# Optimization experiments

Hardware: AMD Instinct MI355X
Metric: run time of the kernel (lower is better)

The kernel has to match this reference:

```python
import jax, jax.numpy as jnp
import numpy as np

N_DELAYS = 512
N_SAMPLES = 2 ** 15  # 32768


def _interp_linear(x, out_size):
    # F.interpolate(mode='linear', align_corners=False) on [B, C, L]
    L = x.shape[-1]
    scale = L / out_size
    pos = (jnp.arange(out_size, dtype=jnp.float32) + 0.5) * scale - 0.5
    pos = jnp.clip(pos, 0.0, L - 1)
    i0 = jnp.floor(pos).astype(jnp.int32)
    i1 = jnp.minimum(i0 + 1, L - 1)
    w = (pos - i0).astype(x.dtype)
    return x[..., i0] * (1.0 - w) + x[..., i1] * w


def _interp_nearest(x, out_size):
    # F.interpolate(mode='nearest') on [B, C, L]: idx = floor(j * L/out)
    L = x.shape[-1]
    idx = jnp.clip(jnp.floor(jnp.arange(out_size) * (L / out_size)).astype(jnp.int32), 0, L - 1)
    return x[..., idx]


def setup_inputs() -> dict:
    key = jax.random.key(0)
    k1, k2, k3, k4, k5 = jax.random.split(key, 5)
    batch = 8
    impulse = jax.random.normal(k1, (batch, 128), dtype=jnp.float32)
    delay_selection = jax.random.normal(k2, (batch, N_DELAYS, 16), dtype=jnp.float32)
    damping = jax.random.normal(k3, (batch, 1), dtype=jnp.float32)
    filt = jax.random.normal(k4, (batch, 16), dtype=jnp.float32)
    # torch forward draws uniform(-1,1) noise; passed as input for determinism
    noise = jax.random.uniform(k5, (batch, 1, N_SAMPLES), dtype=jnp.float32, minval=-1.0, maxval=1.0)
    # comb-filter buffer: delays[i, ::i+1] = 1
    delays_np = np.zeros((N_DELAYS, N_SAMPLES), dtype=np.float32)
    for i in range(N_DELAYS):
        delays_np[i, ::i + 1] = 1.0
    delays = jnp.asarray(delays_np)
    return {"impulse": impulse, "delay_selection": delay_selection, "damping": damping,
            "filt": filt, "noise": noise, "delays": delays}


def reference(impulse, delay_selection, damping, filt, noise, delays):
    batch = delay_selection.shape[0]
    n_delays, n_samples = delays.shape
    n_frames = filt.shape[-1]

    # filter spectrum envelope: sigmoid -> linear upsample to n_samples//2 -> pad 1
    f = jax.nn.sigmoid(filt).reshape(-1, 1, n_frames)
    f = _interp_linear(f, n_samples // 2)
    filt_spec = jnp.pad(f, ((0, 0), (0, 0), (0, 1)))  # [B,1,n_samples//2+1]

    # impulse: squared envelope upsampled, modulating uniform noise
    imp = impulse.reshape(batch, 1, -1) ** 2
    imp = _interp_linear(imp, n_samples) * noise  # [B,1,n_samples]

    # damping: powers = linspace(1, 1, n_frames) == ones (faithful to source)
    damp = jax.nn.sigmoid(damping.reshape(batch, 1)) * 0.9999
    powers = jnp.linspace(1.0, float(damp.shape[-1]), n_frames)
    damp = damp[:, :, None] ** powers[None, None, :]  # [B,1,n_frames]
    damp = _interp_nearest(damp, n_samples)  # [B,1,n_samples]

    # sparse comb selection: softmax over delays, nearest upsample, weighted sum
    ds = jax.nn.softmax(delay_selection.reshape(batch, n_delays, -1), axis=1)
    ds = _interp_nearest(ds, n_samples)  # [B,n_delays,n_samples]
    d = jnp.einsum('bdn,dn->bn', ds, delays)[:, None, :] * damp  # [B,1,n_samples]

    # FFT convolution
    delay_spec = jnp.fft.rfft(d, axis=-1, norm='ortho')
    impulse_spec = jnp.fft.rfft(imp, axis=-1, norm='ortho')
    spec = delay_spec * impulse_spec * filt_spec
    final = jnp.fft.irfft(spec, n=n_samples, axis=-1, norm='ortho')
    return final
```

## Files before the change

### kernel.cpp

```cpp
#include <hip/hip_runtime.h>
#include <math.h>

#define NSAMP 32768
#define NDEL  512
#define NFR   16
#define BATCH 8
#define TWO_PI 6.283185307179586f

__device__ __forceinline__ float2 cmul(float2 a, float2 b) {
    return make_float2(a.x*b.x - a.y*b.y, a.x*b.y + a.y*b.x);
}
__device__ __forceinline__ float2 cadd(float2 a, float2 b){ return make_float2(a.x+b.x, a.y+b.y); }
__device__ __forceinline__ float2 csub(float2 a, float2 b){ return make_float2(a.x-b.x, a.y-b.y); }
__device__ __forceinline__ float2 crot(float2 z, float sign){ return make_float2(-sign*z.y, sign*z.x); }

__device__ __forceinline__ int phi(int i){ return i + (i >> 3); }

__device__ __forceinline__ void bfly8(const float2 v[8], float sign, float2 X[8]) {
    const float S2 = 0.70710678118654752f;
    float2 t0 = cadd(v[0], v[4]), t1 = csub(v[0], v[4]);
    float2 t2 = cadd(v[2], v[6]), t3 = crot(csub(v[2], v[6]), sign);
    float2 E0 = cadd(t0, t2), E1 = cadd(t1, t3), E2 = csub(t0, t2), E3 = csub(t1, t3);
    float2 u0 = cadd(v[1], v[5]), u1 = csub(v[1], v[5]);
    float2 u2 = cadd(v[3], v[7]), u3 = crot(csub(v[3], v[7]), sign);
    float2 O0 = cadd(u0, u2), O1 = cadd(u1, u3), O2 = csub(u0, u2), O3 = csub(u1, u3);
    float2 c1 = make_float2( S2, sign*S2);
    float2 c3 = make_float2(-S2, sign*S2);
    float2 w1o = cmul(c1, O1);
    float2 w2o = crot(O2, sign);
    float2 w3o = cmul(c3, O3);
    X[0]=cadd(E0,O0);  X[4]=csub(E0,O0);
    X[1]=cadd(E1,w1o); X[5]=csub(E1,w1o);
    X[2]=cadd(E2,w2o); X[6]=csub(E2,w2o);
    X[3]=cadd(E3,w3o); X[7]=csub(E3,w3o);
}

__device__ __forceinline__ void twiddle_q(float2 v[8], float ang1) {
    float sa, ca; __sincosf(ang1, &sa, &ca);
    float2 w1 = make_float2(ca, sa), wq = w1;
#pragma unroll
    for (int q = 1; q < 8; ++q) { v[q] = cmul(v[q], wq); wq = cmul(wq, w1); }
}

__global__ void build_kernel(const float* __restrict__ impulse,
                             const float* __restrict__ dsel,
                             const float* __restrict__ damping,
                             const float* __restrict__ noise,
                             float2* __restrict__ At) {
    const int w   = threadIdx.x >> 6;
    const int tid = threadIdx.x & 63;
    const int wid = blockIdx.x * 4 + w;
    const int b   = wid >> 6;
    const int f   = (wid >> 2) & 15;
    const int sub = wid & 3;
    __shared__ float Wrow[4][NDEL];
    __shared__ float dl[4][512];

    float v[8], m = -1e30f;
#pragma unroll
    for (int k = 0; k < 8; ++k) {
        v[k] = dsel[(b*NDEL + tid + 64*k)*NFR + f];
        m = fmaxf(m, v[k]);
    }
#pragma unroll
    for (int off = 1; off < 64; off <<= 1) m = fmaxf(m, __shfl_xor(m, off));
    float e[8], s = 0.0f;
#pragma unroll
    for (int k = 0; k < 8; ++k) { e[k] = __expf(v[k] - m); s += e[k]; }
#pragma unroll
    for (int off = 1; off < 64; off <<= 1) s += __shfl_xor(s, off);

    float damp = 1.0f/(1.0f + __expf(-damping[b])) * 0.9999f;
    float scale = damp / s;
#pragma unroll
    for (int k = 0; k < 8; ++k) Wrow[w][tid + 64*k] = e[k] * scale;
    for (int k = tid; k < 512; k += 64) dl[w][k] = 0.0f;
    __syncthreads();

    const unsigned start = ((unsigned)f << 11) + ((unsigned)sub << 9);
    const float fstart = (float)start;

    for (unsigned t = 1; t < 64; ++t) {
        float wt = Wrow[w][t-1];
        unsigned q0 = (unsigned)(__fdividef(fstart, (float)t));
        unsigned n0 = q0 * t;
        while (n0 < start) n0 += t;
        while (n0 >= start + t) n0 -= t;
        for (unsigned i = (n0 - start) + (unsigned)tid * t; i < 512u; i += 64u * t)
            atomicAdd(&dl[w][i], wt);
    }
    for (unsigned t = 64u + (unsigned)tid; t <= 512u; t += 64u) {
        float wt = Wrow[w][t-1];
        unsigned q0 = (unsigned)(__fdividef(fstart, (float)t));
        unsigned n0 = q0 * t;
        while (n0 < start) n0 += t;
        while (n0 >= start + t) n0 -= t;
        for (unsigned i = n0 - start; i < 512u; i += t)
            atomicAdd(&dl[w][i], wt);
    }
    __syncthreads();

    const int n1base = (int)(start >> 6);
    float2* op = At + b*NSAMP + tid*512 + n1base;
#pragma unroll
    for (int q = 0; q < 8; ++q) {
        int n = (int)start + tid + 64*q;
        float pos = (n + 0.5f) * (1.0f/256.0f) - 0.5f;
        pos = fminf(fmaxf(pos, 0.0f), 127.0f);
        int i0 = (int)pos;
        float w2 = pos - (float)i0;
        int i1 = (i0 + 1 > 127) ? 127 : i0 + 1;
        float x0 = impulse[b*128 + i0]; x0 *= x0;
        float x1 = impulse[b*128 + i1]; x1 *= x1;
        float iv = (x0*(1.0f - w2) + x1*w2) * noise[b*NSAMP + n];
        op[q] = make_float2(dl[w][tid + 64*q], iv);
    }
}

__global__ void fft512_fwd_kernel(const float2* __restrict__ src,
                                  float2* __restrict__ dst) {
    const int w  = threadIdx.x >> 6;
    const int j  = threadIdx.x & 63;
    const int wid = blockIdx.x * 4 + w;
    const int s  = wid >> 6;
    const int n2 = wid & 63;
    __shared__ float2 buf[4][2][576];
    const float sign = -1.0f;

    const float2* sp = src + s * NSAMP;
    float2 v[8], X[8];
#pragma unroll
    for (int q = 0; q < 8; ++q) v[q] = sp[n2*512 + j + 64*q];

    bfly8(v, sign, X);
#pragma unroll
    for (int r = 0; r < 8; ++r) buf[w][0][phi(8*j + r)] = X[r];
    __syncthreads();
#pragma unroll
    for (int q = 0; q < 8; ++q) v[q] = buf[w][0][phi(j + 64*q)];
    int jm = j & 7;
    twiddle_q(v, sign * TWO_PI * (float)jm * (1.0f/64.0f));
    bfly8(v, sign, X);
#pragma unroll
    for (int r = 0; r < 8; ++r) buf[w][1][phi(((j>>3)<<6) + jm + (r<<3))] = X[r];
    __syncthreads();
#pragma unroll
    for (int q = 0; q < 8; ++q) v[q] = buf[w][1][phi(j + 64*q)];
    twiddle_q(v, sign * TWO_PI * (float)j * (1.0f/512.0f));
    bfly8(v, sign, X);

    float2* dp = dst + s * NSAMP + n2 * 512;
#pragma unroll
    for (int r = 0; r < 8; ++r) {
        int k1 = j + 64*r;
        int pr = (n2 * k1) & (NSAMP - 1);
        float sa, ca; __sincosf(sign * TWO_PI * (float)pr * (1.0f/32768.0f), &sa, &ca);
        dp[k1] = cmul(X[r], make_float2(ca, sa));
    }
}

__global__ void mega_kernel(const float2* __restrict__ G,
                            float2* __restrict__ H,
                            const float* __restrict__ filt) {
    const int w  = threadIdx.x >> 6;
    const int l  = threadIdx.x & 63;
    const int cc = l & 7, jj = l >> 3;
    const int s  = blockIdx.x >> 4;
    const int g  = (blockIdx.x & 15) * 4 + w;
    __shared__ float2 Z[4][8][65];
    __shared__ float2 buf[4][576];
    __shared__ float fs[NFR];
    __shared__ int cols[4][8];

    if (threadIdx.x < NFR) fs[threadIdx.x] = 1.0f/(1.0f + __expf(-filt[s*NFR + threadIdx.x]));
    if (l < 8) {
        int col;
        if (l < 4)        col = 4*g + l;
        else if (g == 0)  col = (l == 4) ? 256 : 512 - (l - 4);
        else              col = 512 - 4*g - (l - 4);
        cols[w][l] = col;
    }
    __syncthreads();

    const float2* sp = G + s * NSAMP;
    const int mycol = cols[w][cc];
    float2 v[8], X[8];

#pragma unroll
    for (int q = 0; q < 8; ++q) v[q] = sp[(jj + 8*q)*512 + mycol];
    bfly8(v, -1.0f, X);
#pragma unroll
    for (int r = 0; r < 8; ++r) buf[w][phi(cc*64 + jj*8 + r)] = X[r];
    __syncthreads();
#pragma unroll
    for (int q = 0; q < 8; ++q) v[q] = buf[w][phi(cc*64 + jj + 8*q)];
    twiddle_q(v, -TWO_PI * (float)jj * (1.0f/64.0f));
    bfly8(v, -1.0f, X);
#pragma unroll
    for (int r = 0; r < 8; ++r) Z[w][cc][jj + 8*r] = X[r];
    __syncthreads();

    const float SCALE = 1.0f / (32768.0f * 181.01933598375618f);
#pragma unroll
    for (int it = 0; it < 4; ++it) {
        int c  = l & 3;
        int k2 = (l >> 2) + 16*it;
        if (!(g == 0 && c == 0)) {
            int col = cols[w][c];
            float2 Zk = Z[w][c][k2];
            float2 Zr = Z[w][c+4][63 - k2];
            float2 Zrc = make_float2(Zr.x, -Zr.y);
            float2 D = make_float2(0.5f*(Zk.x + Zrc.x), 0.5f*(Zk.y + Zrc.y));
            float2 df = make_float2(Zk.x - Zrc.x, Zk.y - Zrc.y);
            float2 I = make_float2(0.5f*df.y, -0.5f*df.x);
            int k = col + 512*k2;
            int jjb = (k <= NSAMP - k) ? k : NSAMP - k;
            float fv = 0.0f;
            if (jjb < NSAMP/2) {
                float pos = (jjb + 0.5f) * (1.0f/1024.0f) - 0.5f;
                pos = fminf(fmaxf(pos, 0.0f), 15.0f);
                int i0 = (int)pos;
                float w2 = pos - (float)i0;
                int i1 = (i0 + 1 > 15) ? 15 : i0 + 1;
                fv = fs[i0]*(1.0f - w2) + fs[i1]*w2;
            }
            float2 spec = cmul(D, I);
            float gs = fv * SCALE;
            Z[w][c][k2]        = make_float2( spec.x*gs,  spec.y*gs);
            Z[w][c+4][63 - k2] = make_float2( spec.x*gs, -spec.y*gs);
        }
    }
    if (g == 0) {
        if (l <= 32) {
            int k2 = l, k2p = (64 - k2) & 63;
            float2 Zk = Z[w][0][k2];
            float2 Zr = Z[w][0][k2p];
            float2 Zrc = make_float2(Zr.x, -Zr.y);
            float2 D = make_float2(0.5f*(Zk.x + Zrc.x), 0.5f*(Zk.y + Zrc.y));
            float2 df = make_float2(Zk.x - Zrc.x, Zk.y - Zrc.y);
            float2 I = make_float2(0.5f*df.y, -0.5f*df.x);
            int k = 512*k2;
            int jjb = (k <= NSAMP - k) ? k : NSAMP - k;
            float fv = 0.0f;
            if (jjb < NSAMP/2) {
                float pos = (jjb + 0.5f) * (1.0f/1024.0f) - 0.5f;
                pos = fminf(fmaxf(pos, 0.0f), 15.0f);
                int i0 = (int)pos;
                float w2 = pos - (float)i0;
                int i1 = (i0 + 1 > 15) ? 15 : i0 + 1;
                fv = fs[i0]*(1.0f - w2) + fs[i1]*w2;
            }
            float2 spec = cmul(D, I);
            float gs = fv * SCALE;
            Z[w][0][k2]  = make_float2( spec.x*gs,  spec.y*gs);
            Z[w][0][k2p] = make_float2( spec.x*gs, -spec.y*gs);
        }
        if (l < 32) {
            int k2 = l, k2p = 63 - k2;
            float2 Zk = Z[w][4][k2];
            float2 Zr = Z[w][4][k2p];
            float2 Zrc = make_float2(Zr.x, -Zr.y);
            float2 D = make_float2(0.5f*(Zk.x + Zrc.x), 0.5f*(Zk.y + Zrc.y));
            float2 df = make_float2(Zk.x - Zrc.x, Zk.y - Zrc.y);
            float2 I = make_float2(0.5f*df.y, -0.5f*df.x);
            int k = 256 + 512*k2;
            int jjb = (k <= NSAMP - k) ? k : NSAMP - k;
            float fv = 0.0f;
            {
                float pos = (jjb + 0.5f) * (1.0f/1024.0f) - 0.5f;
                pos = fminf(fmaxf(pos, 0.0f), 15.0f);
                int i0 = (int)pos;
                float w2 = pos - (float)i0;
                int i1 = (i0 + 1 > 15) ? 15 : i0 + 1;
                fv = fs[i0]*(1.0f - w2) + fs[i1]*w2;
            }
            float2 spec = cmul(D, I);
            float gs = fv * SCALE;
            Z[w][4][k2]  = make_float2( spec.x*gs,  spec.y*gs);
            Z[w][4][k2p] = make_float2( spec.x*gs, -spec.y*gs);
        }
    }
    __syncthreads();

#pragma unroll
    for (int q = 0; q < 8; ++q) v[q] = Z[w][cc][jj + 8*q];
    bfly8(v, 1.0f, X);
#pragma unroll
    for (int r = 0; r < 8; ++r) buf[w][phi(cc*64 + jj*8 + r)] = X[r];
    __syncthreads();
#pragma unroll
    for (int q = 0; q < 8; ++q) v[q] = buf[w][phi(cc*64 + jj + 8*q)];
    twiddle_q(v, TWO_PI * (float)jj * (1.0f/64.0f));
    bfly8(v, 1.0f, X);

    float2* hp = H + s * NSAMP + mycol;
#pragma unroll
    for (int r = 0; r < 8; ++r) {
        int n2 = jj + 8*r;
        int pr = (n2 * mycol) & (NSAMP - 1);
        float sa, ca; __sincosf(TWO_PI * (float)pr * (1.0f/32768.0f), &sa, &ca);
        hp[n2*512] = cmul(X[r], make_float2(ca, sa));
    }
}

__global__ void fft512_out_kernel(const float2* __restrict__ H,
                                  float* __restrict__ out) {
    const int w  = threadIdx.x >> 6;
    const int j  = threadIdx.x & 63;
    const int wid = blockIdx.x * 4 + w;
    const int s  = wid >> 6;
    const int n2 = wid & 63;
    __shared__ float2 buf[4][2][576];
    const float sign = 1.0f;

    const float2* sp = H + s * NSAMP;
    float2 v[8], X[8];
#pragma unroll
    for (int q = 0; q < 8; ++q) v[q] = sp[n2*512 + j + 64*q];

    bfly8(v, sign, X);
#pragma unroll
    for (int r = 0; r < 8; ++r) buf[w][0][phi(8*j + r)] = X[r];
    __syncthreads();
#pragma unroll
    for (int q = 0; q < 8; ++q) v[q] = buf[w][0][phi(j + 64*q)];
    int jm = j & 7;
    twiddle_q(v, sign * TWO_PI * (float)jm * (1.0f/64.0f));
    bfly8(v, sign, X);
#pragma unroll
    for (int r = 0; r < 8; ++r) buf[w][1][phi(((j>>3)<<6) + jm + (r<<3))] = X[r];
    __syncthreads();
#pragma unroll
    for (int q = 0; q < 8; ++q) v[q] = buf[w][1][phi(j + 64*q)];
    twiddle_q(v, sign * TWO_PI * (float)j * (1.0f/512.0f));
    bfly8(v, sign, X);

    float* op = out + s * NSAMP + n2;
#pragma unroll
    for (int r = 0; r < 8; ++r) op[64*j + 4096*r] = X[r].x;
}

extern "C" void kernel_launch(void* const* d_in, const int* in_sizes, int n_in,
                              void* d_out, int out_size, void* d_ws, size_t ws_size,
                              hipStream_t stream) {
    const float* impulse = (const float*)d_in[0];
    const float* dsel    = (const float*)d_in[1];
    const float* damping = (const float*)d_in[2];
    const float* filt    = (const float*)d_in[3];
    const float* noise   = (const float*)d_in[4];
    float* out = (float*)d_out;

    float2* A = (float2*)d_ws;
    float2* B = A + BATCH * NSAMP;

    build_kernel     <<<dim3(128), dim3(256), 0, stream>>>(impulse, dsel, damping, noise, A);
    fft512_fwd_kernel<<<dim3(128), dim3(256), 0, stream>>>(A, B);
    mega_kernel      <<<dim3(128), dim3(256), 0, stream>>>(B, A, filt);
    fft512_out_kernel<<<dim3(128), dim3(256), 0, stream>>>(A, out);
}
```

Measured before the change: 138.4 us.

## Fuse four stage kernels into one persistent kernel with software grid barriers

Merges the build, forward FFT, spectral multiply and inverse FFT kernels into one launch of 512 single-wave blocks, separated by an atomic-counter grid barrier. The aim is to remove the launch gaps between four small kernels. It relies on all 512 blocks being resident at once, and the barrier has a timeout that could silently break correctness if they are not. Switching from 4-wave blocks to 1-wave blocks also changes how work is spread across CUs.

```diff
diff --git a/kernel.cpp b/kernel.cpp
--- a/kernel.cpp
+++ b/kernel.cpp
@@ -42,302 +42,321 @@
     for (int q = 1; q < 8; ++q) { v[q] = cmul(v[q], wq); wq = cmul(wq, w1); }
 }
 
-__global__ void build_kernel(const float* __restrict__ impulse,
-                             const float* __restrict__ dsel,
-                             const float* __restrict__ damping,
-                             const float* __restrict__ noise,
-                             float2* __restrict__ At) {
-    const int w   = threadIdx.x >> 6;
-    const int tid = threadIdx.x & 63;
-    const int wid = blockIdx.x * 4 + w;
-    const int b   = wid >> 6;
-    const int f   = (wid >> 2) & 15;
-    const int sub = wid & 3;
-    __shared__ float Wrow[4][NDEL];
-    __shared__ float dl[4][512];
-
-    float v[8], m = -1e30f;
-#pragma unroll
-    for (int k = 0; k < 8; ++k) {
-        v[k] = dsel[(b*NDEL + tid + 64*k)*NFR + f];
-        m = fmaxf(m, v[k]);
-    }
-#pragma unroll
-    for (int off = 1; off < 64; off <<= 1) m = fmaxf(m, __shfl_xor(m, off));
-    float e[8], s = 0.0f;
-#pragma unroll
-    for (int k = 0; k < 8; ++k) { e[k] = __expf(v[k] - m); s += e[k]; }
-#pragma unroll
-    for (int off = 1; off < 64; off <<= 1) s += __shfl_xor(s, off);
-
-    float damp = 1.0f/(1.0f + __expf(-damping[b])) * 0.9999f;
-    float scale = damp / s;
-#pragma unroll
-    for (int k = 0; k < 8; ++k) Wrow[w][tid + 64*k] = e[k] * scale;
-    for (int k = tid; k < 512; k += 64) dl[w][k] = 0.0f;
+__device__ unsigned g_bar = 0;
+
+__device__ __forceinline__ void grid_barrier() {
     __syncthreads();
-
-    const unsigned start = ((unsigned)f << 11) + ((unsigned)sub << 9);
-    const float fstart = (float)start;
-
-    for (unsigned t = 1; t < 64; ++t) {
-        float wt = Wrow[w][t-1];
-        unsigned q0 = (unsigned)(__fdividef(fstart, (float)t));
-        unsigned n0 = q0 * t;
-        while (n0 < start) n0 += t;
-        while (n0 >= start + t) n0 -= t;
-        for (unsigned i = (n0 - start) + (unsigned)tid * t; i < 512u; i += 64u * t)
-            atomicAdd(&dl[w][i], wt);
-    }
-    for (unsigned t = 64u + (unsigned)tid; t <= 512u; t += 64u) {
-        float wt = Wrow[w][t-1];
-        unsigned q0 = (unsigned)(__fdividef(fstart, (float)t));
-        unsigned n0 = q0 * t;
-        while (n0 < start) n0 += t;
-        while (n0 >= start + t) n0 -= t;
-        for (unsigned i = n0 - start; i < 512u; i += t)
-            atomicAdd(&dl[w][i], wt);
+    if (threadIdx.x == 0) {
+        __threadfence();
+        unsigned old = __hip_atomic_fetch_add(&g_bar, 1u, __ATOMIC_ACQ_REL,
+                                              __HIP_MEMORY_SCOPE_AGENT);
+        unsigned tgt = (old & ~511u) + 512u;
+        unsigned tries = 0;
+        while (__hip_atomic_load(&g_bar, __ATOMIC_RELAXED,
+                                 __HIP_MEMORY_SCOPE_AGENT) < tgt) {
+            __builtin_amdgcn_s_sleep(1);
+            if (++tries > 1000000u) break;
+        }
+        __threadfence();
     }
     __syncthreads();
-
-    const int n1base = (int)(start >> 6);
-    float2* op = At + b*NSAMP + tid*512 + n1base;
-#pragma unroll
-    for (int q = 0; q < 8; ++q) {
-        int n = (int)start + tid + 64*q;
-        float pos = (n + 0.5f) * (1.0f/256.0f) - 0.5f;
-        pos = fminf(fmaxf(pos, 0.0f), 127.0f);
-        int i0 = (int)pos;
-        float w2 = pos - (float)i0;
-        int i1 = (i0 + 1 > 127) ? 127 : i0 + 1;
-        float x0 = impulse[b*128 + i0]; x0 *= x0;
-        float x1 = impulse[b*128 + i1]; x1 *= x1;
-        float iv = (x0*(1.0f - w2) + x1*w2) * noise[b*NSAMP + n];
-        op[q] = make_float2(dl[w][tid + 64*q], iv);
-    }
-}
-
-__global__ void fft512_fwd_kernel(const float2* __restrict__ src,
-                                  float2* __restrict__ dst) {
-    const int w  = threadIdx.x >> 6;
-    const int j  = threadIdx.x & 63;
-    const int wid = blockIdx.x * 4 + w;
-    const int s  = wid >> 6;
-    const int n2 = wid & 63;
-    __shared__ float2 buf[4][2][576];
-    const float sign = -1.0f;
-
-    const float2* sp = src + s * NSAMP;
-    float2 v[8], X[8];
-#pragma unroll
-    for (int q = 0; q < 8; ++q) v[q] = sp[n2*512 + j + 64*q];
-
-    bfly8(v, sign, X);
-#pragma unroll
-    for (int r = 0; r < 8; ++r) buf[w][0][phi(8*j + r)] = X[r];
-    __syncthreads();
-#pragma unroll
-    for (int q = 0; q < 8; ++q) v[q] = buf[w][0][phi(j + 64*q)];
-    int jm = j & 7;
-    twiddle_q(v, sign * TWO_PI * (float)jm * (1.0f/64.0f));
-    bfly8(v, sign, X);
-#pragma unroll
-    for (int r = 0; r < 8; ++r) buf[w][1][phi(((j>>3)<<6) + jm + (r<<3))] = X[r];
-    __syncthreads();
-#pragma unroll
-    for (int q = 0; q < 8; ++q) v[q] = buf[w][1][phi(j + 64*q)];
-    twiddle_q(v, sign * TWO_PI * (float)j * (1.0f/512.0f));
-    bfly8(v, sign, X);
-
-    float2* dp = dst + s * NSAMP + n2 * 512;
-#pragma unroll
-    for (int r = 0; r < 8; ++r) {
-        int k1 = j + 64*r;
-        int pr = (n2 * k1) & (NSAMP - 1);
-        float sa, ca; __sincosf(sign * TWO_PI * (float)pr * (1.0f/32768.0f), &sa, &ca);
-        dp[k1] = cmul(X[r], make_float2(ca, sa));
-    }
-}
-
-__global__ void mega_kernel(const float2* __restrict__ G,
-                            float2* __restrict__ H,
-                            const float* __restrict__ filt) {
-    const int w  = threadIdx.x >> 6;
-    const int l  = threadIdx.x & 63;
-    const int cc = l & 7, jj = l >> 3;
-    const int s  = blockIdx.x >> 4;
-    const int g  = (blockIdx.x & 15) * 4 + w;
-    __shared__ float2 Z[4][8][65];
-    __shared__ float2 buf[4][576];
-    __shared__ float fs[NFR];
-    __shared__ int cols[4][8];
-
-    if (threadIdx.x < NFR) fs[threadIdx.x] = 1.0f/(1.0f + __expf(-filt[s*NFR + threadIdx.x]));
-    if (l < 8) {
-        int col;
-        if (l < 4)        col = 4*g + l;
-        else if (g == 0)  col = (l == 4) ? 256 : 512 - (l - 4);
-        else              col = 512 - 4*g - (l - 4);
-        cols[w][l] = col;
-    }
-    __syncthreads();
-
-    const float2* sp = G + s * NSAMP;
-    const int mycol = cols[w][cc];
-    float2 v[8], X[8];
-
-#pragma unroll
-    for (int q = 0; q < 8; ++q) v[q] = sp[(jj + 8*q)*512 + mycol];
-    bfly8(v, -1.0f, X);
-#pragma unroll
-    for (int r = 0; r < 8; ++r) buf[w][phi(cc*64 + jj*8 + r)] = X[r];
-    __syncthreads();
-#pragma unroll
-    for (int q = 0; q < 8; ++q) v[q] = buf[w][phi(cc*64 + jj + 8*q)];
-    twiddle_q(v, -TWO_PI * (float)jj * (1.0f/64.0f));
-    bfly8(v, -1.0f, X);
-#pragma unroll
-    for (int r = 0; r < 8; ++r) Z[w][cc][jj + 8*r] = X[r];
-    __syncthreads();
-
-    const float SCALE = 1.0f / (32768.0f * 181.01933598375618f);
-#pragma unroll
-    for (int it = 0; it < 4; ++it) {
-        int c  = l & 3;
-        int k2 = (l >> 2) + 16*it;
-        if (!(g == 0 && c == 0)) {
-            int col = cols[w][c];
-            float2 Zk = Z[w][c][k2];
-            float2 Zr = Z[w][c+4][63 - k2];
-            float2 Zrc = make_float2(Zr.x, -Zr.y);
-            float2 D = make_float2(0.5f*(Zk.x + Zrc.x), 0.5f*(Zk.y + Zrc.y));
-            float2 df = make_float2(Zk.x - Zrc.x, Zk.y - Zrc.y);
-            float2 I = make_float2(0.5f*df.y, -0.5f*df.x);
-            int k = col + 512*k2;
-            int jjb = (k <= NSAMP - k) ? k : NSAMP - k;
-            float fv = 0.0f;
-            if (jjb < NSAMP/2) {
-                float pos = (jjb + 0.5f) * (1.0f/1024.0f) - 0.5f;
-                pos = fminf(fmaxf(pos, 0.0f), 15.0f);
-                int i0 = (int)pos;
-                float w2 = pos - (float)i0;
-                int i1 = (i0 + 1 > 15) ? 15 : i0 + 1;
-                fv = fs[i0]*(1.0f - w2) + fs[i1]*w2;
+}
+
+__global__ void __launch_bounds__(64) mono_kernel(
+        const float* __restrict__ impulse,
+        const float* __restrict__ dsel,
+        const float* __restrict__ damping,
+        const float* __restrict__ filt,
+        const float* __restrict__ noise,
+        float2* __restrict__ A,
+        float2* __restrict__ B,
+        float* __restrict__ out) {
+    const int tid = threadIdx.x;
+    const int wid = blockIdx.x;
+
+    __shared__ union {
+        struct { float Wrow[NDEL]; float dl[512]; } bs;
+        struct { float2 buf[2][576]; } fs;
+        struct { float2 Z[8][65]; float2 buf[576];
+                 float fsig[NFR]; int cols[8]; } ms;
+    } u;
+
+    {
+        const int b   = wid >> 6;
+        const int f   = (wid >> 2) & 15;
+        const int sub = wid & 3;
+
+        float v[8], m = -1e30f;
+#pragma unroll
+        for (int k = 0; k < 8; ++k) {
+            v[k] = dsel[(b*NDEL + tid + 64*k)*NFR + f];
+            m = fmaxf(m, v[k]);
+        }
+#pragma unroll
+        for (int off = 1; off < 64; off <<= 1) m = fmaxf(m, __shfl_xor(m, off));
+        float e[8], s = 0.0f;
+#pragma unroll
+        for (int k = 0; k < 8; ++k) { e[k] = __expf(v[k] - m); s += e[k]; }
+#pragma unroll
+        for (int off = 1; off < 64; off <<= 1) s += __shfl_xor(s, off);
+
+        float damp = 1.0f/(1.0f + __expf(-damping[b])) * 0.9999f;
+        float scale = damp / s;
+#pragma unroll
+        for (int k = 0; k < 8; ++k) u.bs.Wrow[tid + 64*k] = e[k] * scale;
+        for (int k = tid; k < 512; k += 64) u.bs.dl[k] = 0.0f;
+        __syncthreads();
+
+        const unsigned start = ((unsigned)f << 11) + ((unsigned)sub << 9);
+        const float fstart = (float)start;
+
+        for (unsigned t = 1; t < 64; ++t) {
+            float wt = u.bs.Wrow[t-1];
+            unsigned q0 = (unsigned)(__fdividef(fstart, (float)t));
+            unsigned n0 = q0 * t;
+            while (n0 < start) n0 += t;
+            while (n0 >= start + t) n0 -= t;
+            for (unsigned i = (n0 - start) + (unsigned)tid * t; i < 512u; i += 64u * t)
+                atomicAdd(&u.bs.dl[i], wt);
+        }
+        for (unsigned t = 64u + (unsigned)tid; t <= 512u; t += 64u) {
+            float wt = u.bs.Wrow[t-1];
+            unsigned q0 = (unsigned)(__fdividef(fstart, (float)t));
+            unsigned n0 = q0 * t;
+            while (n0 < start) n0 += t;
+            while (n0 >= start + t) n0 -= t;
+            for (unsigned i = n0 - start; i < 512u; i += t)
+                atomicAdd(&u.bs.dl[i], wt);
+        }
+        __syncthreads();
+
+        const int n1base = (int)(start >> 6);
+        float2* op = A + b*NSAMP + tid*512 + n1base;
+#pragma unroll
+        for (int q = 0; q < 8; ++q) {
+            int n = (int)start + tid + 64*q;
+            float pos = (n + 0.5f) * (1.0f/256.0f) - 0.5f;
+            pos = fminf(fmaxf(pos, 0.0f), 127.0f);
+            int i0 = (int)pos;
+            float w2 = pos - (float)i0;
+            int i1 = (i0 + 1 > 127) ? 127 : i0 + 1;
+            float x0 = impulse[b*128 + i0]; x0 *= x0;
+            float x1 = impulse[b*128 + i1]; x1 *= x1;
+            float iv = (x0*(1.0f - w2) + x1*w2) * noise[b*NSAMP + n];
+            op[q] = make_float2(u.bs.dl[tid + 64*q], iv);
+        }
+    }
+    grid_barrier();
+
+    {
+        const int j  = tid;
+        const int s  = wid >> 6;
+        const int n2 = wid & 63;
+        const float sign = -1.0f;
+
+        const float2* sp = A + s * NSAMP;
+        float2 v[8], X[8];
+#pragma unroll
+        for (int q = 0; q < 8; ++q) v[q] = sp[n2*512 + j + 64*q];
+
+        bfly8(v, sign, X);
+#pragma unroll
+        for (int r = 0; r < 8; ++r) u.fs.buf[0][phi(8*j + r)] = X[r];
+        __syncthreads();
+#pragma unroll
+        for (int q = 0; q < 8; ++q) v[q] = u.fs.buf[0][phi(j + 64*q)];
+        int jm = j & 7;
+        twiddle_q(v, sign * TWO_PI * (float)jm * (1.0f/64.0f));
+        bfly8(v, sign, X);
+#pragma unroll
+        for (int r = 0; r < 8; ++r) u.fs.buf[1][phi(((j>>3)<<6) + jm + (r<<3))] = X[r];
+        __syncthreads();
+#pragma unroll
+        for (int q = 0; q < 8; ++q) v[q] = u.fs.buf[1][phi(j + 64*q)];
+        twiddle_q(v, sign * TWO_PI * (float)j * (1.0f/512.0f));
+        bfly8(v, sign, X);
+
+        float2* dp = B + s * NSAMP + n2 * 512;
+#pragma unroll
+        for (int r = 0; r < 8; ++r) {
+            int k1 = j + 64*r;
+            int pr = (n2 * k1) & (NSAMP - 1);
+            float sa, ca; __sincosf(sign * TWO_PI * (float)pr * (1.0f/32768.0f), &sa, &ca);
+            dp[k1] = cmul(X[r], make_float2(ca, sa));
+        }
+    }
+    grid_barrier();
+
+    {
+        const int l  = tid;
+        const int cc = l & 7, jj = l >> 3;
+        const int s  = wid >> 6;
+        const int g  = wid & 63;
+
+        if (l < NFR) u.ms.fsig[l] = 1.0f/(1.0f + __expf(-filt[s*NFR + l]));
+        if (l < 8) {
+            int col;
+            if (l < 4)        col = 4*g + l;
+            else if (g == 0)  col = (l == 4) ? 256 : 512 - (l - 4);
+            else              col = 512 - 4*g - (l - 4);
+            u.ms.cols[l] = col;
+        }
+        __syncthreads();
+
+        const float2* sp = B + s * NSAMP;
+        const int mycol = u.ms.cols[cc];
+        float2 v[8], X[8];
+
+#pragma unroll
+        for (int q = 0; q < 8; ++q) v[q] = sp[(jj + 8*q)*512 + mycol];
+        bfly8(v, -1.0f, X);
+#pragma unroll
+        for (int r = 0; r < 8; ++r) u.ms.buf[phi(cc*64 + jj*8 + r)] = X[r];
+        __syncthreads();
+#pragma unroll
+        for (int q = 0; q < 8; ++q) v[q] = u.ms.buf[phi(cc*64 + jj + 8*q)];
+        twiddle_q(v, -TWO_PI * (float)jj * (1.0f/64.0f));
+        bfly8(v, -1.0f, X);
+#pragma unroll
+        for (int r = 0; r < 8; ++r) u.ms.Z[cc][jj + 8*r] = X[r];
+        __syncthreads();
+
+        const float SCALE = 1.0f / (32768.0f * 181.01933598375618f);
+#pragma unroll
+        for (int it = 0; it < 4; ++it) {
+            int c  = l & 3;
+            int k2 = (l >> 2) + 16*it;
+            if (!(g == 0 && c == 0)) {
+                int col = u.ms.cols[c];
+                float2 Zk = u.ms.Z[c][k2];
+                float2 Zr = u.ms.Z[c+4][63 - k2];
+                float2 Zrc = make_float2(Zr.x, -Zr.y);
+                float2 D = make_float2(0.5f*(Zk.x + Zrc.x), 0.5f*(Zk.y + Zrc.y));
+                float2 df = make_float2(Zk.x - Zrc.x, Zk.y - Zrc.y);
+                float2 I = make_float2(0.5f*df.y, -0.5f*df.x);
+                int k = col + 512*k2;
+                int jjb = (k <= NSAMP - k) ? k : NSAMP - k;
+                float fv = 0.0f;
+                if (jjb < NSAMP/2) {
+                    float pos = (jjb + 0.5f) * (1.0f/1024.0f) - 0.5f;
+                    pos = fminf(fmaxf(pos, 0.0f), 15.0f);
+                    int i0 = (int)pos;
+                    float w2 = pos - (float)i0;
+                    int i1 = (i0 + 1 > 15) ? 15 : i0 + 1;
+                    fv = u.ms.fsig[i0]*(1.0f - w2) + u.ms.fsig[i1]*w2;
+                }
+                float2 spec = cmul(D, I);
+                float gs = fv * SCALE;
+                u.ms.Z[c][k2]        = make_float2( spec.x*gs,  spec.y*gs);
+                u.ms.Z[c+4][63 - k2] = make_float2( spec.x*gs, -spec.y*gs);
             }
-            float2 spec = cmul(D, I);
-            float gs = fv * SCALE;
-            Z[w][c][k2]        = make_float2( spec.x*gs,  spec.y*gs);
-            Z[w][c+4][63 - k2] = make_float2( spec.x*gs, -spec.y*gs);
-        }
-    }
-    if (g == 0) {
-        if (l <= 32) {
-            int k2 = l, k2p = (64 - k2) & 63;
-            float2 Zk = Z[w][0][k2];
-            float2 Zr = Z[w][0][k2p];
-            float2 Zrc = make_float2(Zr.x, -Zr.y);
-            float2 D = make_float2(0.5f*(Zk.x + Zrc.x), 0.5f*(Zk.y + Zrc.y));
-            float2 df = make_float2(Zk.x - Zrc.x, Zk.y - Zrc.y);
-            float2 I = make_float2(0.5f*df.y, -0.5f*df.x);
-            int k = 512*k2;
-            int jjb = (k <= NSAMP - k) ? k : NSAMP - k;
-            float fv = 0.0f;
-            if (jjb < NSAMP/2) {
-                float pos = (jjb + 0.5f) * (1.0f/1024.0f) - 0.5f;
-                pos = fminf(fmaxf(pos, 0.0f), 15.0f);
-                int i0 = (int)pos;
-                float w2 = pos - (float)i0;
-                int i1 = (i0 + 1 > 15) ? 15 : i0 + 1;
-                fv = fs[i0]*(1.0f - w2) + fs[i1]*w2;
+        }
+        if (g == 0) {
+            if (l <= 32) {
+                int k2 = l, k2p = (64 - k2) & 63;
+                float2 Zk = u.ms.Z[0][k2];
+                float2 Zr = u.ms.Z[0][k2p];
+                float2 Zrc = make_float2(Zr.x, -Zr.y);
+                float2 D = make_float2(0.5f*(Zk.x + Zrc.x), 0.5f*(Zk.y + Zrc.y));
+                float2 df = make_float2(Zk.x - Zrc.x, Zk.y - Zrc.y);
+                float2 I = make_float2(0.5f*df.y, -0.5f*df.x);
+                int k = 512*k2;
+                int jjb = (k <= NSAMP - k) ? k : NSAMP - k;
+                float fv = 0.0f;
+                if (jjb < NSAMP/2) {
+                    float pos = (jjb + 0.5f) * (1.0f/1024.0f) - 0.5f;
+                    pos = fminf(fmaxf(pos, 0.0f), 15.0f);
+                    int i0 = (int)pos;
+                    float w2 = pos - (float)i0;
+                    int i1 = (i0 + 1 > 15) ? 15 : i0 + 1;
+                    fv = u.ms.fsig[i0]*(1.0f - w2) + u.ms.fsig[i1]*w2;
+                }
+                float2 spec = cmul(D, I);
+                float gs = fv * SCALE;
+                u.ms.Z[0][k2]  = make_float2( spec.x*gs,  spec.y*gs);
+                u.ms.Z[0][k2p] = make_float2( spec.x*gs, -spec.y*gs);
             }
-            float2 spec = cmul(D, I);
-            float gs = fv * SCALE;
-            Z[w][0][k2]  = make_float2( spec.x*gs,  spec.y*gs);
-            Z[w][0][k2p] = make_float2( spec.x*gs, -spec.y*gs);
-        }
-        if (l < 32) {
-            int k2 = l, k2p = 63 - k2;
-            float2 Zk = Z[w][4][k2];
-            float2 Zr = Z[w][4][k2p];
-            float2 Zrc = make_float2(Zr.x, -Zr.y);
-            float2 D = make_float2(0.5f*(Zk.x + Zrc.x), 0.5f*(Zk.y + Zrc.y));
-            float2 df = make_float2(Zk.x - Zrc.x, Zk.y - Zrc.y);
-            float2 I = make_float2(0.5f*df.y, -0.5f*df.x);
-            int k = 256 + 512*k2;
-            int jjb = (k <= NSAMP - k) ? k : NSAMP - k;
-            float fv = 0.0f;
-            {
-                float pos = (jjb + 0.5f) * (1.0f/1024.0f) - 0.5f;
-                pos = fminf(fmaxf(pos, 0.0f), 15.0f);
-                int i0 = (int)pos;
-                float w2 = pos - (float)i0;
-                int i1 = (i0 + 1 > 15) ? 15 : i0 + 1;
-                fv = fs[i0]*(1.0f - w2) + fs[i1]*w2;
+            if (l < 32) {
+                int k2 = l, k2p = 63 - k2;
+                float2 Zk = u.ms.Z[4][k2];
+                float2 Zr = u.ms.Z[4][k2p];
+                float2 Zrc = make_float2(Zr.x, -Zr.y);
+                float2 D = make_float2(0.5f*(Zk.x + Zrc.x), 0.5f*(Zk.y + Zrc.y));
+                float2 df = make_float2(Zk.x - Zrc.x, Zk.y - Zrc.y);
+                float2 I = make_float2(0.5f*df.y, -0.5f*df.x);
+                int k = 256 + 512*k2;
+                int jjb = (k <= NSAMP - k) ? k : NSAMP - k;
+                float fv = 0.0f;
+                {
+                    float pos = (jjb + 0.5f) * (1.0f/1024.0f) - 0.5f;
+                    pos = fminf(fmaxf(pos, 0.0f), 15.0f);
+                    int i0 = (int)pos;
+                    float w2 = pos - (float)i0;
+                    int i1 = (i0 + 1 > 15) ? 15 : i0 + 1;
+                    fv = u.ms.fsig[i0]*(1.0f - w2) + u.ms.fsig[i1]*w2;
+                }
+                float2 spec = cmul(D, I);
+                float gs = fv * SCALE;
+                u.ms.Z[4][k2]  = make_float2( spec.x*gs,  spec.y*gs);
+                u.ms.Z[4][k2p] = make_float2( spec.x*gs, -spec.y*gs);
             }
-            float2 spec = cmul(D, I);
-            float gs = fv * SCALE;
-            Z[w][4][k2]  = make_float2( spec.x*gs,  spec.y*gs);
-            Z[w][4][k2p] = make_float2( spec.x*gs, -spec.y*gs);
-        }
-    }
-    __syncthreads();
-
-#pragma unroll
-    for (int q = 0; q < 8; ++q) v[q] = Z[w][cc][jj + 8*q];
-    bfly8(v, 1.0f, X);
-#pragma unroll
-    for (int r = 0; r < 8; ++r) buf[w][phi(cc*64 + jj*8 + r)] = X[r];
-    __syncthreads();
-#pragma unroll
-    for (int q = 0; q < 8; ++q) v[q] = buf[w][phi(cc*64 + jj + 8*q)];
-    twiddle_q(v, TWO_PI * (float)jj * (1.0f/64.0f));
-    bfly8(v, 1.0f, X);
-
-    float2* hp = H + s * NSAMP + mycol;
-#pragma unroll
-    for (int r = 0; r < 8; ++r) {
-        int n2 = jj + 8*r;
-        int pr = (n2 * mycol) & (NSAMP - 1);
-        float sa, ca; __sincosf(TWO_PI * (float)pr * (1.0f/32768.0f), &sa, &ca);
-        hp[n2*512] = cmul(X[r], make_float2(ca, sa));
-    }
-}
-
-__global__ void fft512_out_kernel(const float2* __restrict__ H,
-                                  float* __restrict__ out) {
-    const int w  = threadIdx.x >> 6;
-    const int j  = threadIdx.x & 63;
-    const int wid = blockIdx.x * 4 + w;
-    const int s  = wid >> 6;
-    const int n2 = wid & 63;
-    __shared__ float2 buf[4][2][576];
-    const float sign = 1.0f;
-
-    const float2* sp = H + s * NSAMP;
-    float2 v[8], X[8];
-#pragma unroll
-    for (int q = 0; q < 8; ++q) v[q] = sp[n2*512 + j + 64*q];
-
-    bfly8(v, sign, X);
-#pragma unroll
-    for (int r = 0; r < 8; ++r) buf[w][0][phi(8*j + r)] = X[r];
-    __syncthreads();
-#pragma unroll
-    for (int q = 0; q < 8; ++q) v[q] = buf[w][0][phi(j + 64*q)];
-    int jm = j & 7;
-    twiddle_q(v, sign * TWO_PI * (float)jm * (1.0f/64.0f));
-    bfly8(v, sign, X);
-#pragma unroll
-    for (int r = 0; r < 8; ++r) buf[w][1][phi(((j>>3)<<6) + jm + (r<<3))] = X[r];
-    __syncthreads();
-#pragma unroll
-    for (int q = 0; q < 8; ++q) v[q] = buf[w][1][phi(j + 64*q)];
-    twiddle_q(v, sign * TWO_PI * (float)j * (1.0f/512.0f));
-    bfly8(v, sign, X);
-
-    float* op = out + s * NSAMP + n2;
-#pragma unroll
-    for (int r = 0; r < 8; ++r) op[64*j + 4096*r] = X[r].x;
+        }
+        __syncthreads();
+
+#pragma unroll
+        for (int q = 0; q < 8; ++q) v[q] = u.ms.Z[cc][jj + 8*q];
+        bfly8(v, 1.0f, X);
+#pragma unroll
+        for (int r = 0; r < 8; ++r) u.ms.buf[phi(cc*64 + jj*8 + r)] = X[r];
+        __syncthreads();
+#pragma unroll
+        for (int q = 0; q < 8; ++q) v[q] = u.ms.buf[phi(cc*64 + jj + 8*q)];
+        twiddle_q(v, TWO_PI * (float)jj * (1.0f/64.0f));
+        bfly8(v, 1.0f, X);
+
+        float2* hp = A + s * NSAMP + mycol;
+#pragma unroll
+        for (int r = 0; r < 8; ++r) {
+            int n2 = jj + 8*r;
+            int pr = (n2 * mycol) & (NSAMP - 1);
+            float sa, ca; __sincosf(TWO_PI * (float)pr * (1.0f/32768.0f), &sa, &ca);
+            hp[n2*512] = cmul(X[r], make_float2(ca, sa));
+        }
+    }
+    grid_barrier();
+
+    {
+        const int j  = tid;
+        const int s  = wid >> 6;
+        const int n2 = wid & 63;
+        const float sign = 1.0f;
+
+        const float2* sp = A + s * NSAMP;
+        float2 v[8], X[8];
+#pragma unroll
+        for (int q = 0; q < 8; ++q) v[q] = sp[n2*512 + j + 64*q];
+
+        bfly8(v, sign, X);
+#pragma unroll
+        for (int r = 0; r < 8; ++r) u.fs.buf[0][phi(8*j + r)] = X[r];
+        __syncthreads();
+#pragma unroll
+        for (int q = 0; q < 8; ++q) v[q] = u.fs.buf[0][phi(j + 64*q)];
+        int jm = j & 7;
+        twiddle_q(v, sign * TWO_PI * (float)jm * (1.0f/64.0f));
+        bfly8(v, sign, X);
+#pragma unroll
+        for (int r = 0; r < 8; ++r) u.fs.buf[1][phi(((j>>3)<<6) + jm + (r<<3))] = X[r];
+        __syncthreads();
+#pragma unroll
+        for (int q = 0; q < 8; ++q) v[q] = u.fs.buf[1][phi(j + 64*q)];
+        twiddle_q(v, sign * TWO_PI * (float)j * (1.0f/512.0f));
+        bfly8(v, sign, X);
+
+        float* op = out + s * NSAMP + n2;
+#pragma unroll
+        for (int r = 0; r < 8; ++r) op[64*j + 4096*r] = X[r].x;
+    }
 }
 
 extern "C" void kernel_launch(void* const* d_in, const int* in_sizes, int n_in,
@@ -353,8 +372,6 @@
     float2* A = (float2*)d_ws;
     float2* B = A + BATCH * NSAMP;
 
-    build_kernel     <<<dim3(128), dim3(256), 0, stream>>>(impulse, dsel, damping, noise, A);
-    fft512_fwd_kernel<<<dim3(128), dim3(256), 0, stream>>>(A, B);
-    mega_kernel      <<<dim3(128), dim3(256), 0, stream>>>(B, A, filt);
-    fft512_out_kernel<<<dim3(128), dim3(256), 0, stream>>>(A, out);
-}
+    mono_kernel<<<dim3(512), dim3(64), 0, stream>>>(impulse, dsel, damping,
+                                                    filt, noise, A, B, out);
+}
```

Measured after the change: 281.4 us. 103% more time.
